# Performance work log

Hardware: AMD Instinct MI355X
Metric: run time of the kernel (lower is better)

Reference implementation:

```python
import jax, jax.numpy as jnp
import numpy as np

B = 2; D0 = 41; H = 200; W = 176
C_IN = 128; C_MID = 64
N_PER = 15000; N = B * N_PER
EPS = 1e-3  # spconv BatchNorm1d eps=0.001


def bn_relu(x, valid, gamma, beta):
    # BatchNorm1d (training mode) over ACTIVE voxels only, then ReLU; invalid rows zeroed
    m = valid.astype(x.dtype)[:, None]
    cnt = jnp.maximum(m.sum(), 1.0)
    mean = (x * m).sum(0) / cnt
    var = (((x - mean) ** 2) * m).sum(0) / cnt
    y = gamma * (x - mean) * jax.lax.rsqrt(var + EPS) + beta
    return jnp.maximum(y, 0.0) * m


def build_idx_map(coords, valid, D):
    # dense voxel -> row-index map (-1 = inactive); invalid rows routed out-of-bounds and dropped
    n = coords.shape[0]
    oob = jnp.array([B, D, H, W], jnp.int32)
    c = jnp.where(valid[:, None], coords, oob)
    idx = jnp.full((B, D, H, W), -1, jnp.int32)
    return idx.at[c[:, 0], c[:, 1], c[:, 2], c[:, 3]].set(
        jnp.arange(n, dtype=jnp.int32), mode='drop')


def subm_conv3(feats, coords, valid, idx_map, weight):
    # submanifold 3x3x3 conv: gather active neighbors, GEMM per kernel offset, accumulate
    D = idx_map.shape[1]
    b, z, y, x = coords[:, 0], coords[:, 1], coords[:, 2], coords[:, 3]
    out = jnp.zeros((feats.shape[0], weight.shape[-1]), feats.dtype)
    for dz in (-1, 0, 1):
        for dy in (-1, 0, 1):
            for dx in (-1, 0, 1):
                nz, ny, nx = z + dz, y + dy, x + dx
                inb = valid & (nz >= 0) & (nz < D) & (ny >= 0) & (ny < H) \
                      & (nx >= 0) & (nx < W)
                j = idx_map[b, jnp.clip(nz, 0, D - 1),
                            jnp.clip(ny, 0, H - 1), jnp.clip(nx, 0, W - 1)]
                ok = inb & (j >= 0)
                g = jnp.where(ok[:, None], feats[jnp.clip(j, 0)], 0.0)
                out = out + g @ weight[dz + 1, dy + 1, dx + 1]
    return out


def sparse_conv_z(feats, coords, valid, D, weight):
    # regular SparseConv3d kernel (3,1,1), stride (2,1,1), pad 0: scatter-GEMM into unique outputs
    Dout = (D - 3) // 2 + 1
    b, z, y, x = coords[:, 0], coords[:, 1], coords[:, 2], coords[:, 3]
    sent = B * Dout * H * W  # sentinel linear id (> any valid id)
    cap = 2 * feats.shape[0] + 1  # each input hits <= 2 outputs, + sentinel slot
    lins, vals = [], []
    for kz in range(3):
        t = z - kz
        oz = t // 2
        ok = valid & (t >= 0) & (t % 2 == 0) & (oz < Dout)
        lin = ((b * Dout + oz) * H + y) * W + x
        lins.append(jnp.where(ok, lin, sent))
        vals.append(feats @ weight[kz])
    lin_all = jnp.concatenate(lins)
    val_all = jnp.concatenate(vals)
    uniq = jnp.unique(lin_all, size=cap, fill_value=sent)
    seg = jnp.searchsorted(uniq, lin_all)
    out = jax.ops.segment_sum(val_all, seg, num_segments=cap)
    new_valid = uniq != sent
    lin = jnp.where(new_valid, uniq, 0)
    nb = lin // (Dout * H * W)
    r = lin % (Dout * H * W)
    nz = r // (H * W)
    ny = (r % (H * W)) // W
    nx = r % W
    new_coords = jnp.stack([nb, nz, ny, nx], 1).astype(jnp.int32)
    return out, new_coords, new_valid, Dout


def forward(voxel_features, coors, batch_size,
            w_subm0, g0, b0, w_s1, gs1, bs1,
            w_subm1a, g1a, b1a, w_subm1b, g1b, b1b, w_s2, gs2, bs2):
    v0 = jnp.ones((voxel_features.shape[0],), bool)
    idx0 = build_idx_map(coors, v0, D0)
    x = subm_conv3(voxel_features, coors, v0, idx0, w_subm0)   # 128 -> 64, subm0
    x = bn_relu(x, v0, g0, b0)
    x, c1, v1, D1 = sparse_conv_z(x, coors, v0, D0, w_s1)      # D: 41 -> 20
    x = bn_relu(x, v1, gs1, bs1)
    idx1 = build_idx_map(c1, v1, D1)
    x = bn_relu(subm_conv3(x, c1, v1, idx1, w_subm1a), v1, g1a, b1a)  # subm1
    x = bn_relu(subm_conv3(x, c1, v1, idx1, w_subm1b), v1, g1b, b1b)
    x, c2, v2, D2 = sparse_conv_z(x, c1, v1, D1, w_s2)         # D: 20 -> 9
    x = bn_relu(x, v2, gs2, bs2)
    oob = jnp.array([B, D2, H, W], jnp.int32)
    c2s = jnp.where(v2[:, None], c2, oob)
    dense = jnp.zeros((B, D2, H, W, C_MID), x.dtype)
    dense = dense.at[c2s[:, 0], c2s[:, 1], c2s[:, 2], c2s[:, 3]].set(x, mode='drop')
    dense = dense.transpose(0, 4, 1, 2, 3)                     # [B, C, D2, H, W]
    return dense.reshape(B, C_MID * D2, H, W)


def setup_inputs() -> dict:
    key = jax.random.key(0)
    ks = jax.random.split(key, 6)
    rng = np.random.default_rng(0)
    rows = []
    for b in range(B):
        lin = rng.choice(D0 * H * W, N_PER, replace=False)
        z = lin // (H * W); y = (lin % (H * W)) // W; x = lin % W
        rows.append(np.stack([np.full(N_PER, b), z, y, x], 1))
    coors = jnp.asarray(np.concatenate(rows), jnp.int32)
    s0 = 1.0 / np.sqrt(27.0 * C_IN)
    s1 = 1.0 / np.sqrt(27.0 * C_MID)
    sz = 1.0 / np.sqrt(3.0 * C_MID)
    ones = jnp.ones((C_MID,), jnp.float32)
    zeros = jnp.zeros((C_MID,), jnp.float32)
    return {
        'voxel_features': jax.random.normal(ks[0], (N, C_IN), jnp.float32),
        'coors': coors,
        'batch_size': B,
        'w_subm0': jax.random.normal(ks[1], (3, 3, 3, C_IN, C_MID), jnp.float32) * s0,
        'g0': ones, 'b0': zeros,
        'w_s1': jax.random.normal(ks[2], (3, C_MID, C_MID), jnp.float32) * sz,
        'gs1': ones, 'bs1': zeros,
        'w_subm1a': jax.random.normal(ks[3], (3, 3, 3, C_MID, C_MID), jnp.float32) * s1,
        'g1a': ones, 'b1a': zeros,
        'w_subm1b': jax.random.normal(ks[4], (3, 3, 3, C_MID, C_MID), jnp.float32) * s1,
        'g1b': ones, 'b1b': zeros,
        'w_s2': jax.random.normal(ks[5], (3, C_MID, C_MID), jnp.float32) * sz,
        'gs2': ones, 'bs2': zeros,
    }


def reference(voxel_features, coors, batch_size,
              w_subm0, g0, b0, w_s1, gs1, bs1,
              w_subm1a, g1a, b1a, w_subm1b, g1b, b1b, w_s2, gs2, bs2):
    return forward(voxel_features, coors, batch_size,
                   w_subm0, g0, b0, w_s1, gs1, bs1,
                   w_subm1a, g1a, b1a, w_subm1b, g1b, b1b, w_s2, gs2, bs2)
```

## Files before the change

### kernel.cpp

```cpp
#include <hip/hip_runtime.h>

typedef unsigned short u16;
typedef unsigned int u32;
typedef unsigned long long u64;
typedef __attribute__((ext_vector_type(8))) short bf16x8;
typedef __attribute__((ext_vector_type(4))) float f32x4;

#define H_ 200
#define W_ 176
#define HW_ (200 * 176)
#define D0_ 41
#define D1_ 20
#define D2_ 9
#define B_ 2

__device__ __forceinline__ u16 f2bf(float f) {
  union { float f; u32 u; } c; c.f = f;
  u32 u = c.u;
  u32 r = (u + 0x7fffu + ((u >> 16) & 1u)) >> 16;
  return (u16)r;
}

struct P {
  const float* feats; const int* coors;
  const float *w0, *w1a, *w1b, *wz1, *wz2;
  const float *g0, *b0, *g1, *b1, *g2, *b2, *g3, *b3, *g4, *b4;
  int* ctrl; float* stats;
  int *idx0, *idx1, *claim2;
  int* nbr1; u32* gmask1;
  int *nbrz1, *nbrz2, *coords1, *coords2;
  float *xb0, *xb1, *xb2, *xb3, *xb4;
  u16 *fb, *wf0, *wf1a, *wf1b, *wfz1, *wfz2;
  float* out;
  uint4* fillp;
  int N, nfill16;
  long prepTotal;
};

__device__ __forceinline__ void repack1(const float* __restrict__ w, u16* __restrict__ frag,
                                        int K, int t) {
  int j = t & 7;
  int lane = (t >> 3) & 63;
  int nt = (t >> 9) & 3;
  int rest = t >> 11;
  int KS = K / 32;
  int ks = rest % KS;
  int o = rest / KS;
  int k = ks * 32 + (lane >> 4) * 8 + j;
  int n = nt * 16 + (lane & 15);
  frag[t] = f2bf(w[((size_t)o * K + k) * 64 + n]);
}

__device__ __forceinline__ void claim_ep(int t, int base, int width, int cnt,
                                         const int* __restrict__ coordsIn,
                                         const int* __restrict__ idxin, int Din, int Dout,
                                         int* __restrict__ claim, int* __restrict__ coords_out,
                                         int* __restrict__ nbrzN, int* __restrict__ outcnt) {
  int i = base + t;
  bool w0 = false, w1 = false;
  int pos0 = 0, pos1 = 0, oz0 = -1, oz1 = -1;
  int b = 0, z = 0, yy = 0, xx = 0;
  if (t < width && i < cnt) {
    int4 cc = *(const int4*)(coordsIn + (size_t)i * 4);
    b = cc.x; z = cc.y; yy = cc.z; xx = cc.w;
    if (z & 1) {
      int oz = (z - 1) >> 1;
      if (oz < Dout) oz0 = oz;
    } else {
      int oz = z >> 1;
      if (oz < Dout) oz0 = oz;
      if (z >= 2) oz1 = oz - 1;
    }
    if (oz0 >= 0) {
      pos0 = ((b * Dout + oz0) * H_ + yy) * W_ + xx;
      w0 = (atomicCAS(&claim[pos0], -1, -2) == -1);
    }
    if (oz1 >= 0) {
      pos1 = ((b * Dout + oz1) * H_ + yy) * W_ + xx;
      w1 = (atomicCAS(&claim[pos1], -1, -2) == -1);
    }
  }
  u64 m0 = __ballot(w0), m1 = __ballot(w1);
  int c0 = __popcll(m0), c1 = __popcll(m1);
  int lane = t & 63;
  u64 lt = (lane == 63) ? 0x7FFFFFFFFFFFFFFFull : ((1ull << lane) - 1ull);
  int bse2 = 0;
  if (lane == 0 && (c0 + c1) > 0) bse2 = atomicAdd(outcnt, c0 + c1);
  bse2 = __shfl(bse2, 0);
  if (w0) {
    int id = bse2 + __popcll(m0 & lt);
    claim[pos0] = id;
    coords_out[id * 4 + 0] = b; coords_out[id * 4 + 1] = oz0;
    coords_out[id * 4 + 2] = yy; coords_out[id * 4 + 3] = xx;
    size_t bse = ((size_t)(b * Din + 2 * oz0) * H_ + yy) * W_ + xx;
    nbrzN[id * 3 + 0] = idxin[bse];
    nbrzN[id * 3 + 1] = idxin[bse + HW_];
    nbrzN[id * 3 + 2] = idxin[bse + 2 * (size_t)HW_];
  }
  if (w1) {
    int id = bse2 + c0 + __popcll(m1 & lt);
    claim[pos1] = id;
    coords_out[id * 4 + 0] = b; coords_out[id * 4 + 1] = oz1;
    coords_out[id * 4 + 2] = yy; coords_out[id * 4 + 3] = xx;
    size_t bse = ((size_t)(b * Din + 2 * oz1) * H_ + yy) * W_ + xx;
    nbrzN[id * 3 + 0] = idxin[bse];
    nbrzN[id * 3 + 1] = idxin[bse + HW_];
    nbrzN[id * 3 + 2] = idxin[bse + 2 * (size_t)HW_];
  }
}

__device__ __forceinline__ void bn_pre(const float* __restrict__ statsIn, int cntN,
                                       const float* __restrict__ gamma,
                                       const float* __restrict__ beta,
                                       float* __restrict__ ggs, float* __restrict__ bbs, int t) {
  if (t < 64) {
    float s = 0.f, q = 0.f;
#pragma unroll
    for (int k = 0; k < 4; ++k) { s += statsIn[k * 128 + t]; q += statsIn[k * 128 + 64 + t]; }
    float cf = (float)(cntN > 0 ? cntN : 1);
    float mean = s / cf;
    float var = q / cf - mean * mean;
    float inv = rsqrtf(var + 1e-3f);
    float g = gamma[t] * inv;
    ggs[t] = g;
    bbs[t] = beta[t] - mean * g;
  }
}

__device__ __forceinline__ void buildA64(const float* __restrict__ xp, int j, int kr,
                                         const float* gr_, const float* br_, bf16x8* aa) {
  if (j >= 0) {
    const float* src = xp + (size_t)j * 64 + kr * 8;
#pragma unroll
    for (int ks = 0; ks < 2; ++ks) {
      float4 v0 = *(const float4*)(src + ks * 32);
      float4 v1 = *(const float4*)(src + ks * 32 + 4);
      bf16x8 w;
      w[0] = (short)f2bf(fmaxf(v0.x * gr_[ks * 8 + 0] + br_[ks * 8 + 0], 0.f));
      w[1] = (short)f2bf(fmaxf(v0.y * gr_[ks * 8 + 1] + br_[ks * 8 + 1], 0.f));
      w[2] = (short)f2bf(fmaxf(v0.z * gr_[ks * 8 + 2] + br_[ks * 8 + 2], 0.f));
      w[3] = (short)f2bf(fmaxf(v0.w * gr_[ks * 8 + 3] + br_[ks * 8 + 3], 0.f));
      w[4] = (short)f2bf(fmaxf(v1.x * gr_[ks * 8 + 4] + br_[ks * 8 + 4], 0.f));
      w[5] = (short)f2bf(fmaxf(v1.y * gr_[ks * 8 + 5] + br_[ks * 8 + 5], 0.f));
      w[6] = (short)f2bf(fmaxf(v1.z * gr_[ks * 8 + 6] + br_[ks * 8 + 6], 0.f));
      w[7] = (short)f2bf(fmaxf(v1.w * gr_[ks * 8 + 7] + br_[ks * 8 + 7], 0.f));
      aa[ks] = w;
    }
  } else {
    bf16x8 zf = {0, 0, 0, 0, 0, 0, 0, 0};
    aa[0] = zf; aa[1] = zf;
  }
}

template <int KS>
__device__ __forceinline__ void mfma_step(const u16* __restrict__ bw, const bf16x8* a,
                                          f32x4& acc0, f32x4& acc1, f32x4& acc2, f32x4& acc3) {
#pragma unroll
  for (int ks = 0; ks < KS; ++ks) {
    const u16* bwk = bw + ks * 2048;
    acc0 = __builtin_amdgcn_mfma_f32_16x16x32_bf16(a[ks], *(const bf16x8*)(bwk), acc0, 0, 0, 0);
    acc1 = __builtin_amdgcn_mfma_f32_16x16x32_bf16(a[ks], *(const bf16x8*)(bwk + 512), acc1, 0, 0, 0);
    acc2 = __builtin_amdgcn_mfma_f32_16x16x32_bf16(a[ks], *(const bf16x8*)(bwk + 1024), acc2, 0, 0, 0);
    acc3 = __builtin_amdgcn_mfma_f32_16x16x32_bf16(a[ks], *(const bf16x8*)(bwk + 1536), acc3, 0, 0, 0);
  }
}

__device__ __forceinline__ void store_stats64(int base, int cnt, int am, int kr,
                                              const f32x4& acc0, const f32x4& acc1,
                                              const f32x4& acc2, const f32x4& acc3,
                                              float* __restrict__ out,
                                              float* __restrict__ lsum, float* __restrict__ lss) {
  float s0 = 0.f, s1 = 0.f, s2 = 0.f, s3 = 0.f;
  float q0 = 0.f, q1 = 0.f, q2 = 0.f, q3 = 0.f;
#pragma unroll
  for (int r = 0; r < 4; ++r) {
    int po = base + kr * 4 + r;
    if (po < cnt) {
      float* op = out + (size_t)po * 64 + am;
      op[0] = acc0[r]; op[16] = acc1[r]; op[32] = acc2[r]; op[48] = acc3[r];
      s0 += acc0[r]; q0 += acc0[r] * acc0[r];
      s1 += acc1[r]; q1 += acc1[r] * acc1[r];
      s2 += acc2[r]; q2 += acc2[r] * acc2[r];
      s3 += acc3[r]; q3 += acc3[r] * acc3[r];
    }
  }
  atomicAdd(&lsum[am], s0); atomicAdd(&lss[am], q0);
  atomicAdd(&lsum[am + 16], s1); atomicAdd(&lss[am + 16], q1);
  atomicAdd(&lsum[am + 32], s2); atomicAdd(&lss[am + 32], q2);
  atomicAdd(&lsum[am + 48], s3); atomicAdd(&lss[am + 48], q3);
}

__device__ __forceinline__ void flush_stats(int t, int bid, float* __restrict__ statsOut,
                                            const float* __restrict__ lsum,
                                            const float* __restrict__ lss) {
  if (t < 64) {
    float s = lsum[t], q = lss[t];
    if (s != 0.f || q != 0.f) {
      float* dst = statsOut + (bid & 3) * 128;
      atomicAdd(&dst[t], s);
      atomicAdd(&dst[64 + t], q);
    }
  }
}


__global__ void k_s0(P p) {
  long gtid = (long)blockIdx.x * 256 + threadIdx.x;
  long gstride = (long)gridDim.x * 256;
  uint4 v;
  v.x = 0xFFFFFFFFu; v.y = 0xFFFFFFFFu; v.z = 0xFFFFFFFFu; v.w = 0xFFFFFFFFu;
  for (long i = gtid; i < p.nfill16; i += gstride) p.fillp[i] = v;
  for (long i = gtid; i < 2560; i += gstride) p.stats[i] = 0.f;
  if (gtid < 3) p.ctrl[gtid] = (gtid == 0) ? p.N : 0;
}

__global__ void k_s1(P p) {
  long tt = (long)blockIdx.x * 256 + threadIdx.x;
  if (tt >= p.prepTotal) return;
  long NC = (long)p.N * 128;
  if (tt < NC) { p.fb[tt] = f2bf(p.feats[tt]); return; }
  tt -= NC;
  if (tt < 221184) { repack1(p.w0, p.wf0, 128, (int)tt); return; }
  tt -= 221184;
  if (tt < 110592) { repack1(p.w1a, p.wf1a, 64, (int)tt); return; }
  tt -= 110592;
  if (tt < 110592) { repack1(p.w1b, p.wf1b, 64, (int)tt); return; }
  tt -= 110592;
  if (tt < 12288) { repack1(p.wz1, p.wfz1, 64, (int)tt); return; }
  tt -= 12288;
  if (tt < 12288) { repack1(p.wz2, p.wfz2, 64, (int)tt); return; }
  tt -= 12288;
  if (tt < p.N) {
    int i = (int)tt;
    int b = p.coors[i * 4], z = p.coors[i * 4 + 1], y = p.coors[i * 4 + 2], x = p.coors[i * 4 + 3];
    p.idx0[((size_t)(b * D0_ + z) * H_ + y) * W_ + x] = i;
  }
}

__global__ __launch_bounds__(256) void k_conv0(P p) {
  __shared__ int snbr[432];
  __shared__ u32 smaskS;
  __shared__ float accbuf[4][1024];
  __shared__ float lsum[64], lss[64];
  const int t = threadIdx.x;
  const int cnt = p.N;
  const int base = blockIdx.x * 16;
  if (base >= cnt) return;
  const int lane = t & 63, wg = t >> 6, am = lane & 15, kr = lane >> 4;
  if (t == 0) smaskS = 0;
  if (t < 64) { lsum[t] = 0.f; lss[t] = 0.f; }
  __syncthreads();
  for (int r = t; r < 432; r += 256) {
    int o = r >> 4;
    int i = base + (r & 15);
    int j = -1;
    if (i < cnt) {
      int4 cc = *(const int4*)(p.coors + (size_t)i * 4);
      int nz = cc.y + o / 9 - 1, ny = cc.z + (o / 3) % 3 - 1, nx = cc.w + o % 3 - 1;
      if ((u32)nz < (u32)D0_ && (u32)ny < (u32)H_ && (u32)nx < (u32)W_)
        j = p.idx0[((size_t)(cc.x * D0_ + nz) * H_ + ny) * W_ + nx];
    }
    snbr[r] = j;
    if (j >= 0) atomicOr(&smaskS, 1u << o);
  }
  __syncthreads();
  int olist[7], mycnt = 0;
  {
    u32 m = smaskS;
    int idx = 0;
    while (m) {
      int o = __builtin_ctz(m);
      m &= m - 1;
      if ((idx & 3) == wg) olist[mycnt++] = o;
      ++idx;
    }
  }
  f32x4 acc0 = {0.f, 0.f, 0.f, 0.f};
  f32x4 acc1 = acc0, acc2 = acc0, acc3 = acc0;
  bf16x8 zf = {0, 0, 0, 0, 0, 0, 0, 0};
  bf16x8 a[4], an[4];
  if (mycnt) {
    int j = snbr[olist[0] * 16 + am];
#pragma unroll
    for (int ks = 0; ks < 4; ++ks)
      a[ks] = (j >= 0) ? *(const bf16x8*)(p.fb + (size_t)j * 128 + ks * 32 + kr * 8) : zf;
    for (int ii = 0; ii < mycnt; ++ii) {
      int jn = (ii + 1 < mycnt) ? snbr[olist[ii + 1] * 16 + am] : -1;
#pragma unroll
      for (int ks = 0; ks < 4; ++ks)
        an[ks] = (jn >= 0) ? *(const bf16x8*)(p.fb + (size_t)jn * 128 + ks * 32 + kr * 8) : zf;
      mfma_step<4>(p.wf0 + (size_t)olist[ii] * 8192 + lane * 8, a, acc0, acc1, acc2, acc3);
#pragma unroll
      for (int ks = 0; ks < 4; ++ks) a[ks] = an[ks];
    }
  }
#pragma unroll
  for (int r = 0; r < 4; ++r) {
    int pi = kr * 4 + r;
    accbuf[wg][pi * 64 + am] = acc0[r];
    accbuf[wg][pi * 64 + am + 16] = acc1[r];
    accbuf[wg][pi * 64 + am + 32] = acc2[r];
    accbuf[wg][pi * 64 + am + 48] = acc3[r];
  }
  __syncthreads();
  for (int e = t; e < 1024; e += 256) {
    int pi = e >> 6, c = e & 63;
    float v = accbuf[0][e] + accbuf[1][e] + accbuf[2][e] + accbuf[3][e];
    if (base + pi < cnt) {
      p.xb0[(size_t)(base + pi) * 64 + c] = v;
      atomicAdd(&lsum[c], v);
      atomicAdd(&lss[c], v * v);
    }
  }
  __syncthreads();
  if (t < 64) {
    flush_stats(t, blockIdx.x, p.stats + 0, lsum, lss);
    claim_ep(t, base, 16, cnt, p.coors, p.idx0, D0_, D1_, p.idx1, p.coords1, p.nbrz1, p.ctrl + 1);
  }
}

__global__ __launch_bounds__(256) void k_convz1(P p) {
  const int cnt1 = p.ctrl[1];
  const int blockBase = blockIdx.x * 64;
  if (blockBase >= cnt1) return;
  __shared__ float lsum[64], lss[64], ggs[64], bbs[64];
  __shared__ u32 smask[4];
  const int t = threadIdx.x;
  const int lane = t & 63, wg = t >> 6, am = lane & 15, kr = lane >> 4;
  if (t < 64) { lsum[t] = 0.f; lss[t] = 0.f; }
  if (t < 4) smask[t] = 0;
  bn_pre(p.stats + 0, p.N, p.g0, p.b0, ggs, bbs, t);
  __syncthreads();
  for (int r = t; r < 1728; r += 256) {
    int g = r / 432;
    int rr = r - g * 432;
    int o = rr >> 4;
    int i = blockBase + g * 16 + (rr & 15);
    int j = -1;
    if (i < cnt1) {
      int4 cc = *(const int4*)(p.coords1 + (size_t)i * 4);
      int nz = cc.y + o / 9 - 1, ny = cc.z + (o / 3) % 3 - 1, nx = cc.w + o % 3 - 1;
      if ((u32)nz < (u32)D1_ && (u32)ny < (u32)H_ && (u32)nx < (u32)W_)
        j = p.idx1[((size_t)(cc.x * D1_ + nz) * H_ + ny) * W_ + nx];
    }
    p.nbr1[(size_t)(blockIdx.x * 4 + g) * 432 + rr] = j;
    if (j >= 0) atomicOr(&smask[g], 1u << o);
  }
  __syncthreads();
  if (t < 4) p.gmask1[blockIdx.x * 4 + t] = smask[t];
  float gr_[16], br_[16];
#pragma unroll
  for (int ks = 0; ks < 2; ++ks)
#pragma unroll
    for (int e = 0; e < 8; ++e) {
      int c = ks * 32 + kr * 8 + e;
      gr_[ks * 8 + e] = ggs[c];
      br_[ks * 8 + e] = bbs[c];
    }
  int base = blockBase + wg * 16;
  f32x4 acc0 = {0.f, 0.f, 0.f, 0.f};
  f32x4 acc1 = acc0, acc2 = acc0, acc3 = acc0;
  if (base < cnt1) {
    int pt = base + am;
    bool vpt = pt < cnt1;
    const int* np = p.nbrz1 + (size_t)pt * 3;
    bf16x8 a[2], an[2];
    int j = vpt ? np[0] : -1;
    buildA64(p.xb0, j, kr, gr_, br_, a);
    for (int o = 0; o < 3; ++o) {
      int jn = (o + 1 < 3 && vpt) ? np[o + 1] : -1;
      buildA64(p.xb0, jn, kr, gr_, br_, an);
      mfma_step<2>(p.wfz1 + (size_t)o * 4096 + lane * 8, a, acc0, acc1, acc2, acc3);
      a[0] = an[0]; a[1] = an[1];
    }
    store_stats64(base, cnt1, am, kr, acc0, acc1, acc2, acc3, p.xb1, lsum, lss);
  }
  __syncthreads();
  if (t < 64) {
    flush_stats(t, blockIdx.x, p.stats + 512, lsum, lss);
    claim_ep(t, blockBase, 64, cnt1, p.coords1, p.idx1, D1_, D2_, p.claim2, p.coords2, p.nbrz2,
             p.ctrl + 2);
  }
}

__global__ __launch_bounds__(256) void k_conv1(P p, const float* __restrict__ xin,
                                               float* __restrict__ xout,
                                               const u16* __restrict__ wf,
                                               const float* __restrict__ sIn,
                                               float* __restrict__ sOut,
                                               const float* __restrict__ gam,
                                               const float* __restrict__ bet) {
  __shared__ float accbuf[4][1024];
  __shared__ float lsum[64], lss[64], ggs[64], bbs[64];
  const int cnt1 = p.ctrl[1];
  const int g = blockIdx.x;
  const int base = g * 16;
  if (base >= cnt1) return;
  const int t = threadIdx.x;
  const int lane = t & 63, wg = t >> 6, am = lane & 15, kr = lane >> 4;
  if (t < 64) { lsum[t] = 0.f; lss[t] = 0.f; }
  bn_pre(sIn, cnt1, gam, bet, ggs, bbs, t);
  __syncthreads();
  float gr_[16], br_[16];
#pragma unroll
  for (int ks = 0; ks < 2; ++ks)
#pragma unroll
    for (int e = 0; e < 8; ++e) {
      int c = ks * 32 + kr * 8 + e;
      gr_[ks * 8 + e] = ggs[c];
      br_[ks * 8 + e] = bbs[c];
    }
  const int* nb = p.nbr1 + (size_t)g * 432;
  int olist[7], mycnt = 0;
  {
    u32 m = p.gmask1[g];
    int idx = 0;
    while (m) {
      int o = __builtin_ctz(m);
      m &= m - 1;
      if ((idx & 3) == wg) olist[mycnt++] = o;
      ++idx;
    }
  }
  f32x4 acc0 = {0.f, 0.f, 0.f, 0.f};
  f32x4 acc1 = acc0, acc2 = acc0, acc3 = acc0;
  bf16x8 a[2], an[2];
  if (mycnt) {
    buildA64(xin, nb[olist[0] * 16 + am], kr, gr_, br_, a);
    for (int ii = 0; ii < mycnt; ++ii) {
      int jn = (ii + 1 < mycnt) ? nb[olist[ii + 1] * 16 + am] : -1;
      buildA64(xin, jn, kr, gr_, br_, an);
      mfma_step<2>(wf + (size_t)olist[ii] * 4096 + lane * 8, a, acc0, acc1, acc2, acc3);
      a[0] = an[0]; a[1] = an[1];
    }
  }
#pragma unroll
  for (int r = 0; r < 4; ++r) {
    int pi = kr * 4 + r;
    accbuf[wg][pi * 64 + am] = acc0[r];
    accbuf[wg][pi * 64 + am + 16] = acc1[r];
    accbuf[wg][pi * 64 + am + 32] = acc2[r];
    accbuf[wg][pi * 64 + am + 48] = acc3[r];
  }
  __syncthreads();
  for (int e = t; e < 1024; e += 256) {
    int pi = e >> 6, c = e & 63;
    float v = accbuf[0][e] + accbuf[1][e] + accbuf[2][e] + accbuf[3][e];
    if (base + pi < cnt1) {
      xout[(size_t)(base + pi) * 64 + c] = v;
      atomicAdd(&lsum[c], v);
      atomicAdd(&lss[c], v * v);
    }
  }
  __syncthreads();
  flush_stats(t, blockIdx.x, sOut, lsum, lss);
}

__global__ __launch_bounds__(256) void k_convz2(P p) {
  const int cnt1 = p.ctrl[1];
  const int cnt2 = p.ctrl[2];
  const int blockBase = blockIdx.x * 64;
  if (blockBase >= cnt2) return;
  __shared__ float lsum[64], lss[64], ggs[64], bbs[64];
  const int t = threadIdx.x;
  const int lane = t & 63, wg = t >> 6, am = lane & 15, kr = lane >> 4;
  if (t < 64) { lsum[t] = 0.f; lss[t] = 0.f; }
  bn_pre(p.stats + 1536, cnt1, p.g3, p.b3, ggs, bbs, t);
  __syncthreads();
  float gr_[16], br_[16];
#pragma unroll
  for (int ks = 0; ks < 2; ++ks)
#pragma unroll
    for (int e = 0; e < 8; ++e) {
      int c = ks * 32 + kr * 8 + e;
      gr_[ks * 8 + e] = ggs[c];
      br_[ks * 8 + e] = bbs[c];
    }
  int base = blockBase + wg * 16;
  if (base < cnt2) {
    int pt = base + am;
    bool vpt = pt < cnt2;
    const int* np = p.nbrz2 + (size_t)pt * 3;
    f32x4 acc0 = {0.f, 0.f, 0.f, 0.f};
    f32x4 acc1 = acc0, acc2 = acc0, acc3 = acc0;
    bf16x8 a[2], an[2];
    int j = vpt ? np[0] : -1;
    buildA64(p.xb3, j, kr, gr_, br_, a);
    for (int o = 0; o < 3; ++o) {
      int jn = (o + 1 < 3 && vpt) ? np[o + 1] : -1;
      buildA64(p.xb3, jn, kr, gr_, br_, an);
      mfma_step<2>(p.wfz2 + (size_t)o * 4096 + lane * 8, a, acc0, acc1, acc2, acc3);
      a[0] = an[0]; a[1] = an[1];
    }
    store_stats64(base, cnt2, am, kr, acc0, acc1, acc2, acc3, p.xb4, lsum, lss);
  }
  __syncthreads();
  flush_stats(t, blockIdx.x, p.stats + 2048, lsum, lss);
}

__global__ void k_s7(P p) {
  const int XQ = W_ / 4;
  const int cnt2 = p.ctrl[2];
  const long total = (long)B_ * 64 * D2_ * H_ * XQ;
  long tt = (long)blockIdx.x * 256 + threadIdx.x;
  if (tt >= total) return;
  const float* st = p.stats + 2048;
  int xq = (int)(tt % XQ);
  long row = tt / XQ;
  int y = (int)(row % H_);
  long r2 = row / H_;
  int oz = (int)(r2 % D2_);
  r2 /= D2_;
  int c = (int)(r2 & 63);
  int b = (int)(r2 >> 6);
  float s = 0.f, q = 0.f;
#pragma unroll
  for (int k = 0; k < 4; ++k) { s += st[k * 128 + c]; q += st[k * 128 + 64 + c]; }
  float cf = (float)(cnt2 > 0 ? cnt2 : 1);
  float mean = s / cf;
  float var = q / cf - mean * mean;
  float inv = rsqrtf(var + 1e-3f);
  float g = p.g4[c] * inv;
  float bb = p.b4[c] - mean * g;
  int pos = ((b * D2_ + oz) * H_ + y) * W_ + xq * 4;
  int4 ids = *(const int4*)(p.claim2 + pos);
  float4 v;
  v.x = (ids.x >= 0) ? fmaxf(p.xb4[(size_t)ids.x * 64 + c] * g + bb, 0.f) : 0.f;
  v.y = (ids.y >= 0) ? fmaxf(p.xb4[(size_t)ids.y * 64 + c] * g + bb, 0.f) : 0.f;
  v.z = (ids.z >= 0) ? fmaxf(p.xb4[(size_t)ids.z * 64 + c] * g + bb, 0.f) : 0.f;
  v.w = (ids.w >= 0) ? fmaxf(p.xb4[(size_t)ids.w * 64 + c] * g + bb, 0.f) : 0.f;
  *(float4*)(p.out + (size_t)row * W_ + xq * 4) = v;
}

extern "C" void kernel_launch(void* const* d_in, const int* in_sizes, int n_in,
                              void* d_out, int out_size, void* d_ws, size_t ws_size,
                              hipStream_t stream) {
  const int N = in_sizes[0] / 128;
  const int cap1 = 2 * N + 8;
  const int cap2 = 4 * N + 8;
  const int ng1 = (cap1 + 15) / 16;

  char* ws = (char*)d_ws;
  size_t off = 0;
  auto alloc = [&](size_t bytes) -> void* {
    size_t o = off;
    off = (off + bytes + 255) & ~(size_t)255;
    return (void*)(ws + o);
  };

  P p;
  p.ctrl = (int*)alloc(16);
  p.stats = (float*)alloc(2560 * 4);
  size_t fill_beg = off;
  p.idx0 = (int*)alloc((size_t)B_ * D0_ * HW_ * 4);
  p.idx1 = (int*)alloc((size_t)B_ * D1_ * HW_ * 4);
  p.claim2 = (int*)alloc((size_t)B_ * D2_ * HW_ * 4);
  size_t fill_end = off;
  p.nbr1 = (int*)alloc((size_t)(ng1 + 4) * 432 * 4);
  p.gmask1 = (u32*)alloc((size_t)(ng1 + 4) * 4);
  p.nbrz1 = (int*)alloc((size_t)cap1 * 3 * 4);
  p.nbrz2 = (int*)alloc((size_t)cap2 * 3 * 4);
  p.coords1 = (int*)alloc((size_t)cap1 * 4 * 4);
  p.coords2 = (int*)alloc((size_t)cap2 * 4 * 4);
  p.xb0 = (float*)alloc((size_t)N * 64 * 4);
  p.xb1 = (float*)alloc((size_t)cap1 * 64 * 4);
  p.xb2 = (float*)alloc((size_t)cap1 * 64 * 4);
  p.xb3 = (float*)alloc((size_t)cap1 * 64 * 4);
  p.xb4 = (float*)alloc((size_t)cap2 * 64 * 4);
  p.fb = (u16*)alloc((size_t)N * 128 * 2);
  p.wf0 = (u16*)alloc((size_t)27 * 4 * 2048 * 2);
  p.wf1a = (u16*)alloc((size_t)27 * 2 * 2048 * 2);
  p.wf1b = (u16*)alloc((size_t)27 * 2 * 2048 * 2);
  p.wfz1 = (u16*)alloc((size_t)3 * 2 * 2048 * 2);
  p.wfz2 = (u16*)alloc((size_t)3 * 2 * 2048 * 2);

  p.feats = (const float*)d_in[0];
  p.coors = (const int*)d_in[1];
  p.w0 = (const float*)d_in[3];
  p.g0 = (const float*)d_in[4]; p.b0 = (const float*)d_in[5];
  p.wz1 = (const float*)d_in[6];
  p.g1 = (const float*)d_in[7]; p.b1 = (const float*)d_in[8];
  p.w1a = (const float*)d_in[9];
  p.g2 = (const float*)d_in[10]; p.b2 = (const float*)d_in[11];
  p.w1b = (const float*)d_in[12];
  p.g3 = (const float*)d_in[13]; p.b3 = (const float*)d_in[14];
  p.wz2 = (const float*)d_in[15];
  p.g4 = (const float*)d_in[16]; p.b4 = (const float*)d_in[17];
  p.out = (float*)d_out;
  p.fillp = (uint4*)(ws + fill_beg);
  p.N = N;
  p.nfill16 = (int)((fill_end - fill_beg) / 16);
  p.prepTotal = (long)N * 128 + 221184 + 110592 + 110592 + 12288 + 12288 + N;

  const int ng0 = (N + 15) / 16;
  const int nbz1 = (cap1 + 63) / 64;
  const int nbz2 = (cap2 + 63) / 64;
  const long outThreads = (long)B_ * 64 * D2_ * H_ * (W_ / 4);

  k_s0<<<dim3(512), 256, 0, stream>>>(p);
  k_s1<<<dim3((unsigned)((p.prepTotal + 255) / 256)), 256, 0, stream>>>(p);
  k_conv0<<<dim3(ng0), 256, 0, stream>>>(p);
  k_convz1<<<dim3(nbz1), 256, 0, stream>>>(p);
  k_conv1<<<dim3(ng1), 256, 0, stream>>>(p, p.xb1, p.xb2, p.wf1a, p.stats + 512,
                                         p.stats + 1024, p.g1, p.b1);
  k_conv1<<<dim3(ng1), 256, 0, stream>>>(p, p.xb2, p.xb3, p.wf1b, p.stats + 1024,
                                         p.stats + 1536, p.g2, p.b2);
  k_convz2<<<dim3(nbz2), 256, 0, stream>>>(p);
  k_s7<<<dim3((unsigned)((outThreads + 255) / 256)), 256, 0, stream>>>(p);
}
```

Measured before the change: 432.8 us.

## Give each wave its own 16-point group and batch neighbor gathers four-wide

```diff
diff --git a/kernel.cpp b/kernel.cpp
--- a/kernel.cpp
+++ b/kernel.cpp
@@ -51,7 +51,7 @@
   frag[t] = f2bf(w[((size_t)o * K + k) * 64 + n]);
 }
 
-__device__ __forceinline__ void claim_ep(int t, int base, int width, int cnt,
+__device__ __forceinline__ void claim_ep(int t, int base, int cnt,
                                          const int* __restrict__ coordsIn,
                                          const int* __restrict__ idxin, int Din, int Dout,
                                          int* __restrict__ claim, int* __restrict__ coords_out,
@@ -60,7 +60,7 @@
   bool w0 = false, w1 = false;
   int pos0 = 0, pos1 = 0, oz0 = -1, oz1 = -1;
   int b = 0, z = 0, yy = 0, xx = 0;
-  if (t < width && i < cnt) {
+  if (i < cnt) {
     int4 cc = *(const int4*)(coordsIn + (size_t)i * 4);
     b = cc.x; z = cc.y; yy = cc.z; xx = cc.w;
     if (z & 1) {
@@ -127,14 +127,23 @@
   }
 }
 
-__device__ __forceinline__ void buildA64(const float* __restrict__ xp, int j, int kr,
-                                         const float* gr_, const float* br_, bf16x8* aa) {
+__device__ __forceinline__ void loadRaw64(const float* __restrict__ xp, int j, int kr,
+                                          float4* __restrict__ r) {
   if (j >= 0) {
     const float* src = xp + (size_t)j * 64 + kr * 8;
+    r[0] = *(const float4*)(src);
+    r[1] = *(const float4*)(src + 4);
+    r[2] = *(const float4*)(src + 32);
+    r[3] = *(const float4*)(src + 36);
+  }
+}
+
+__device__ __forceinline__ void cvtA64(const float4* __restrict__ r, int j,
+                                       const float* gr_, const float* br_, bf16x8* aa) {
+  if (j >= 0) {
 #pragma unroll
     for (int ks = 0; ks < 2; ++ks) {
-      float4 v0 = *(const float4*)(src + ks * 32);
-      float4 v1 = *(const float4*)(src + ks * 32 + 4);
+      float4 v0 = r[ks * 2], v1 = r[ks * 2 + 1];
       bf16x8 w;
       w[0] = (short)f2bf(fmaxf(v0.x * gr_[ks * 8 + 0] + br_[ks * 8 + 0], 0.f));
       w[1] = (short)f2bf(fmaxf(v0.y * gr_[ks * 8 + 1] + br_[ks * 8 + 1], 0.f));
@@ -238,21 +247,22 @@
 }
 
 __global__ __launch_bounds__(256) void k_conv0(P p) {
-  __shared__ int snbr[432];
-  __shared__ u32 smaskS;
-  __shared__ float accbuf[4][1024];
+  __shared__ int snbr[1728];
+  __shared__ u32 smask[4];
   __shared__ float lsum[64], lss[64];
   const int t = threadIdx.x;
   const int cnt = p.N;
-  const int base = blockIdx.x * 16;
-  if (base >= cnt) return;
+  const int blockBase = blockIdx.x * 64;
+  if (blockBase >= cnt) return;
   const int lane = t & 63, wg = t >> 6, am = lane & 15, kr = lane >> 4;
-  if (t == 0) smaskS = 0;
   if (t < 64) { lsum[t] = 0.f; lss[t] = 0.f; }
-  __syncthreads();
-  for (int r = t; r < 432; r += 256) {
-    int o = r >> 4;
-    int i = base + (r & 15);
+  if (t < 4) smask[t] = 0;
+  __syncthreads();
+  for (int r = t; r < 1728; r += 256) {
+    int g = r / 432;
+    int rr = r - g * 432;
+    int o = rr >> 4;
+    int i = blockBase + g * 16 + (rr & 15);
     int j = -1;
     if (i < cnt) {
       int4 cc = *(const int4*)(p.coors + (size_t)i * 4);
@@ -261,61 +271,45 @@
         j = p.idx0[((size_t)(cc.x * D0_ + nz) * H_ + ny) * W_ + nx];
     }
     snbr[r] = j;
-    if (j >= 0) atomicOr(&smaskS, 1u << o);
-  }
-  __syncthreads();
-  int olist[7], mycnt = 0;
-  {
-    u32 m = smaskS;
-    int idx = 0;
-    while (m) {
-      int o = __builtin_ctz(m);
-      m &= m - 1;
-      if ((idx & 3) == wg) olist[mycnt++] = o;
-      ++idx;
-    }
-  }
+    if (j >= 0) atomicOr(&smask[g], 1u << o);
+  }
+  __syncthreads();
+  int base = blockBase + wg * 16;
   f32x4 acc0 = {0.f, 0.f, 0.f, 0.f};
   f32x4 acc1 = acc0, acc2 = acc0, acc3 = acc0;
-  bf16x8 zf = {0, 0, 0, 0, 0, 0, 0, 0};
-  bf16x8 a[4], an[4];
-  if (mycnt) {
-    int j = snbr[olist[0] * 16 + am];
-#pragma unroll
-    for (int ks = 0; ks < 4; ++ks)
-      a[ks] = (j >= 0) ? *(const bf16x8*)(p.fb + (size_t)j * 128 + ks * 32 + kr * 8) : zf;
-    for (int ii = 0; ii < mycnt; ++ii) {
-      int jn = (ii + 1 < mycnt) ? snbr[olist[ii + 1] * 16 + am] : -1;
-#pragma unroll
-      for (int ks = 0; ks < 4; ++ks)
-        an[ks] = (jn >= 0) ? *(const bf16x8*)(p.fb + (size_t)jn * 128 + ks * 32 + kr * 8) : zf;
-      mfma_step<4>(p.wf0 + (size_t)olist[ii] * 8192 + lane * 8, a, acc0, acc1, acc2, acc3);
-#pragma unroll
-      for (int ks = 0; ks < 4; ++ks) a[ks] = an[ks];
-    }
-  }
-#pragma unroll
-  for (int r = 0; r < 4; ++r) {
-    int pi = kr * 4 + r;
-    accbuf[wg][pi * 64 + am] = acc0[r];
-    accbuf[wg][pi * 64 + am + 16] = acc1[r];
-    accbuf[wg][pi * 64 + am + 32] = acc2[r];
-    accbuf[wg][pi * 64 + am + 48] = acc3[r];
-  }
-  __syncthreads();
-  for (int e = t; e < 1024; e += 256) {
-    int pi = e >> 6, c = e & 63;
-    float v = accbuf[0][e] + accbuf[1][e] + accbuf[2][e] + accbuf[3][e];
-    if (base + pi < cnt) {
-      p.xb0[(size_t)(base + pi) * 64 + c] = v;
-      atomicAdd(&lsum[c], v);
-      atomicAdd(&lss[c], v * v);
-    }
+  if (base < cnt) {
+    u32 mask = smask[wg];
+    const int* nb = snbr + wg * 432 + am;
+    bf16x8 zf = {0, 0, 0, 0, 0, 0, 0, 0};
+    while (mask) {
+      int os0 = __builtin_ctz(mask); mask &= mask - 1;
+      int os1 = -1, os2 = -1, os3 = -1;
+      if (mask) { os1 = __builtin_ctz(mask); mask &= mask - 1; }
+      if (mask) { os2 = __builtin_ctz(mask); mask &= mask - 1; }
+      if (mask) { os3 = __builtin_ctz(mask); mask &= mask - 1; }
+      int j0 = nb[os0 * 16];
+      int j1 = (os1 >= 0) ? nb[os1 * 16] : -1;
+      int j2 = (os2 >= 0) ? nb[os2 * 16] : -1;
+      int j3 = (os3 >= 0) ? nb[os3 * 16] : -1;
+      bf16x8 a0[4], a1[4], a2[4], a3[4];
+#pragma unroll
+      for (int ks = 0; ks < 4; ++ks) {
+        a0[ks] = (j0 >= 0) ? *(const bf16x8*)(p.fb + (size_t)j0 * 128 + ks * 32 + kr * 8) : zf;
+        a1[ks] = (j1 >= 0) ? *(const bf16x8*)(p.fb + (size_t)j1 * 128 + ks * 32 + kr * 8) : zf;
+        a2[ks] = (j2 >= 0) ? *(const bf16x8*)(p.fb + (size_t)j2 * 128 + ks * 32 + kr * 8) : zf;
+        a3[ks] = (j3 >= 0) ? *(const bf16x8*)(p.fb + (size_t)j3 * 128 + ks * 32 + kr * 8) : zf;
+      }
+      mfma_step<4>(p.wf0 + (size_t)os0 * 8192 + lane * 8, a0, acc0, acc1, acc2, acc3);
+      if (os1 >= 0) mfma_step<4>(p.wf0 + (size_t)os1 * 8192 + lane * 8, a1, acc0, acc1, acc2, acc3);
+      if (os2 >= 0) mfma_step<4>(p.wf0 + (size_t)os2 * 8192 + lane * 8, a2, acc0, acc1, acc2, acc3);
+      if (os3 >= 0) mfma_step<4>(p.wf0 + (size_t)os3 * 8192 + lane * 8, a3, acc0, acc1, acc2, acc3);
+    }
+    store_stats64(base, cnt, am, kr, acc0, acc1, acc2, acc3, p.xb0, lsum, lss);
   }
   __syncthreads();
   if (t < 64) {
     flush_stats(t, blockIdx.x, p.stats + 0, lsum, lss);
-    claim_ep(t, base, 16, cnt, p.coors, p.idx0, D0_, D1_, p.idx1, p.coords1, p.nbrz1, p.ctrl + 1);
+    claim_ep(t, blockBase, cnt, p.coors, p.idx0, D0_, D1_, p.idx1, p.coords1, p.nbrz1, p.ctrl + 1);
   }
 }
 
@@ -364,21 +358,26 @@
     int pt = base + am;
     bool vpt = pt < cnt1;
     const int* np = p.nbrz1 + (size_t)pt * 3;
-    bf16x8 a[2], an[2];
-    int j = vpt ? np[0] : -1;
-    buildA64(p.xb0, j, kr, gr_, br_, a);
-    for (int o = 0; o < 3; ++o) {
-      int jn = (o + 1 < 3 && vpt) ? np[o + 1] : -1;
-      buildA64(p.xb0, jn, kr, gr_, br_, an);
-      mfma_step<2>(p.wfz1 + (size_t)o * 4096 + lane * 8, a, acc0, acc1, acc2, acc3);
-      a[0] = an[0]; a[1] = an[1];
-    }
+    int j0 = vpt ? np[0] : -1;
+    int j1 = vpt ? np[1] : -1;
+    int j2 = vpt ? np[2] : -1;
+    float4 r0[4], r1[4], r2[4];
+    loadRaw64(p.xb0, j0, kr, r0);
+    loadRaw64(p.xb0, j1, kr, r1);
+    loadRaw64(p.xb0, j2, kr, r2);
+    bf16x8 a[2];
+    cvtA64(r0, j0, gr_, br_, a);
+    mfma_step<2>(p.wfz1 + lane * 8, a, acc0, acc1, acc2, acc3);
+    cvtA64(r1, j1, gr_, br_, a);
+    mfma_step<2>(p.wfz1 + 4096 + lane * 8, a, acc0, acc1, acc2, acc3);
+    cvtA64(r2, j2, gr_, br_, a);
+    mfma_step<2>(p.wfz1 + 8192 + lane * 8, a, acc0, acc1, acc2, acc3);
     store_stats64(base, cnt1, am, kr, acc0, acc1, acc2, acc3, p.xb1, lsum, lss);
   }
   __syncthreads();
   if (t < 64) {
     flush_stats(t, blockIdx.x, p.stats + 512, lsum, lss);
-    claim_ep(t, blockBase, 64, cnt1, p.coords1, p.idx1, D1_, D2_, p.claim2, p.coords2, p.nbrz2,
+    claim_ep(t, blockBase, cnt1, p.coords1, p.idx1, D1_, D2_, p.claim2, p.coords2, p.nbrz2,
              p.ctrl + 2);
   }
 }
@@ -390,12 +389,10 @@
                                                float* __restrict__ sOut,
                                                const float* __restrict__ gam,
                                                const float* __restrict__ bet) {
-  __shared__ float accbuf[4][1024];
+  const int cnt1 = p.ctrl[1];
+  const int blockBase = blockIdx.x * 64;
+  if (blockBase >= cnt1) return;
   __shared__ float lsum[64], lss[64], ggs[64], bbs[64];
-  const int cnt1 = p.ctrl[1];
-  const int g = blockIdx.x;
-  const int base = g * 16;
-  if (base >= cnt1) return;
   const int t = threadIdx.x;
   const int lane = t & 63, wg = t >> 6, am = lane & 15, kr = lane >> 4;
   if (t < 64) { lsum[t] = 0.f; lss[t] = 0.f; }
@@ -410,47 +407,45 @@
       gr_[ks * 8 + e] = ggs[c];
       br_[ks * 8 + e] = bbs[c];
     }
-  const int* nb = p.nbr1 + (size_t)g * 432;
-  int olist[7], mycnt = 0;
-  {
-    u32 m = p.gmask1[g];
-    int idx = 0;
-    while (m) {
-      int o = __builtin_ctz(m);
-      m &= m - 1;
-      if ((idx & 3) == wg) olist[mycnt++] = o;
-      ++idx;
-    }
-  }
+  int base = blockBase + wg * 16;
   f32x4 acc0 = {0.f, 0.f, 0.f, 0.f};
   f32x4 acc1 = acc0, acc2 = acc0, acc3 = acc0;
-  bf16x8 a[2], an[2];
-  if (mycnt) {
-    buildA64(xin, nb[olist[0] * 16 + am], kr, gr_, br_, a);
-    for (int ii = 0; ii < mycnt; ++ii) {
-      int jn = (ii + 1 < mycnt) ? nb[olist[ii + 1] * 16 + am] : -1;
-      buildA64(xin, jn, kr, gr_, br_, an);
-      mfma_step<2>(wf + (size_t)olist[ii] * 4096 + lane * 8, a, acc0, acc1, acc2, acc3);
-      a[0] = an[0]; a[1] = an[1];
-    }
-  }
-#pragma unroll
-  for (int r = 0; r < 4; ++r) {
-    int pi = kr * 4 + r;
-    accbuf[wg][pi * 64 + am] = acc0[r];
-    accbuf[wg][pi * 64 + am + 16] = acc1[r];
-    accbuf[wg][pi * 64 + am + 32] = acc2[r];
-    accbuf[wg][pi * 64 + am + 48] = acc3[r];
-  }
-  __syncthreads();
-  for (int e = t; e < 1024; e += 256) {
-    int pi = e >> 6, c = e & 63;
-    float v = accbuf[0][e] + accbuf[1][e] + accbuf[2][e] + accbuf[3][e];
-    if (base + pi < cnt1) {
-      xout[(size_t)(base + pi) * 64 + c] = v;
-      atomicAdd(&lsum[c], v);
-      atomicAdd(&lss[c], v * v);
-    }
+  if (base < cnt1) {
+    int g = blockIdx.x * 4 + wg;
+    u32 mask = p.gmask1[g];
+    const int* nb = p.nbr1 + (size_t)g * 432 + am;
+    bf16x8 a[2];
+    while (mask) {
+      int os0 = __builtin_ctz(mask); mask &= mask - 1;
+      int os1 = -1, os2 = -1, os3 = -1;
+      if (mask) { os1 = __builtin_ctz(mask); mask &= mask - 1; }
+      if (mask) { os2 = __builtin_ctz(mask); mask &= mask - 1; }
+      if (mask) { os3 = __builtin_ctz(mask); mask &= mask - 1; }
+      int j0 = nb[os0 * 16];
+      int j1 = (os1 >= 0) ? nb[os1 * 16] : -1;
+      int j2 = (os2 >= 0) ? nb[os2 * 16] : -1;
+      int j3 = (os3 >= 0) ? nb[os3 * 16] : -1;
+      float4 r0[4], r1[4], r2[4], r3[4];
+      loadRaw64(xin, j0, kr, r0);
+      loadRaw64(xin, j1, kr, r1);
+      loadRaw64(xin, j2, kr, r2);
+      loadRaw64(xin, j3, kr, r3);
+      cvtA64(r0, j0, gr_, br_, a);
+      mfma_step<2>(wf + (size_t)os0 * 4096 + lane * 8, a, acc0, acc1, acc2, acc3);
+      if (os1 >= 0) {
+        cvtA64(r1, j1, gr_, br_, a);
+        mfma_step<2>(wf + (size_t)os1 * 4096 + lane * 8, a, acc0, acc1, acc2, acc3);
+      }
+      if (os2 >= 0) {
+        cvtA64(r2, j2, gr_, br_, a);
+        mfma_step<2>(wf + (size_t)os2 * 4096 + lane * 8, a, acc0, acc1, acc2, acc3);
+      }
+      if (os3 >= 0) {
+        cvtA64(r3, j3, gr_, br_, a);
+        mfma_step<2>(wf + (size_t)os3 * 4096 + lane * 8, a, acc0, acc1, acc2, acc3);
+      }
+    }
+    store_stats64(base, cnt1, am, kr, acc0, acc1, acc2, acc3, xout, lsum, lss);
   }
   __syncthreads();
   flush_stats(t, blockIdx.x, sOut, lsum, lss);
@@ -481,17 +476,22 @@
     int pt = base + am;
     bool vpt = pt < cnt2;
     const int* np = p.nbrz2 + (size_t)pt * 3;
+    int j0 = vpt ? np[0] : -1;
+    int j1 = vpt ? np[1] : -1;
+    int j2 = vpt ? np[2] : -1;
+    float4 r0[4], r1[4], r2[4];
+    loadRaw64(p.xb3, j0, kr, r0);
+    loadRaw64(p.xb3, j1, kr, r1);
+    loadRaw64(p.xb3, j2, kr, r2);
     f32x4 acc0 = {0.f, 0.f, 0.f, 0.f};
     f32x4 acc1 = acc0, acc2 = acc0, acc3 = acc0;
-    bf16x8 a[2], an[2];
-    int j = vpt ? np[0] : -1;
-    buildA64(p.xb3, j, kr, gr_, br_, a);
-    for (int o = 0; o < 3; ++o) {
-      int jn = (o + 1 < 3 && vpt) ? np[o + 1] : -1;
-      buildA64(p.xb3, jn, kr, gr_, br_, an);
-      mfma_step<2>(p.wfz2 + (size_t)o * 4096 + lane * 8, a, acc0, acc1, acc2, acc3);
-      a[0] = an[0]; a[1] = an[1];
-    }
+    bf16x8 a[2];
+    cvtA64(r0, j0, gr_, br_, a);
+    mfma_step<2>(p.wfz2 + lane * 8, a, acc0, acc1, acc2, acc3);
+    cvtA64(r1, j1, gr_, br_, a);
+    mfma_step<2>(p.wfz2 + 4096 + lane * 8, a, acc0, acc1, acc2, acc3);
+    cvtA64(r2, j2, gr_, br_, a);
+    mfma_step<2>(p.wfz2 + 8192 + lane * 8, a, acc0, acc1, acc2, acc3);
     store_stats64(base, cnt2, am, kr, acc0, acc1, acc2, acc3, p.xb4, lsum, lss);
   }
   __syncthreads();
@@ -592,19 +592,19 @@
   p.nfill16 = (int)((fill_end - fill_beg) / 16);
   p.prepTotal = (long)N * 128 + 221184 + 110592 + 110592 + 12288 + 12288 + N;
 
-  const int ng0 = (N + 15) / 16;
-  const int nbz1 = (cap1 + 63) / 64;
-  const int nbz2 = (cap2 + 63) / 64;
+  const int nb0 = (N + 63) / 64;
+  const int nb1 = (cap1 + 63) / 64;
+  const int nb2 = (cap2 + 63) / 64;
   const long outThreads = (long)B_ * 64 * D2_ * H_ * (W_ / 4);
 
   k_s0<<<dim3(512), 256, 0, stream>>>(p);
   k_s1<<<dim3((unsigned)((p.prepTotal + 255) / 256)), 256, 0, stream>>>(p);
-  k_conv0<<<dim3(ng0), 256, 0, stream>>>(p);
-  k_convz1<<<dim3(nbz1), 256, 0, stream>>>(p);
-  k_conv1<<<dim3(ng1), 256, 0, stream>>>(p, p.xb1, p.xb2, p.wf1a, p.stats + 512,
+  k_conv0<<<dim3(nb0), 256, 0, stream>>>(p);
+  k_convz1<<<dim3(nb1), 256, 0, stream>>>(p);
+  k_conv1<<<dim3(nb1), 256, 0, stream>>>(p, p.xb1, p.xb2, p.wf1a, p.stats + 512,
                                          p.stats + 1024, p.g1, p.b1);
-  k_conv1<<<dim3(ng1), 256, 0, stream>>>(p, p.xb2, p.xb3, p.wf1b, p.stats + 1024,
+  k_conv1<<<dim3(nb1), 256, 0, stream>>>(p, p.xb2, p.xb3, p.wf1b, p.stats + 1024,
                                          p.stats + 1536, p.g2, p.b2);
-  k_convz2<<<dim3(nbz2), 256, 0, stream>>>(p);
+  k_convz2<<<dim3(nb2), 256, 0, stream>>>(p);
   k_s7<<<dim3((unsigned)((outThreads + 255) / 256)), 256, 0, stream>>>(p);
 }
```

After: 376.3 us. 13.1% less time.
